# Kernel tuning notes

Measured on AMD Instinct MI355X. Metric: run time of the kernel, lower is better.

The kernel has to match this reference:

```python
import jax, jax.numpy as jnp
import numpy as np

DIM = 1024
HEADS = 16
HEAD_DIM = DIM // HEADS
B, S = 2, 2048


def setup_inputs() -> dict:
    key = jax.random.key(0)
    ks = jax.random.split(key, 12)
    scale = 1.0 / np.sqrt(DIM)
    inp = {
        "Q_in": jax.random.normal(ks[0], (B, S, DIM), jnp.float32),
        "K_in": jax.random.normal(ks[1], (B, S, DIM), jnp.float32),
        "V_in": jax.random.normal(ks[2], (B, S, DIM), jnp.float32),
        "Wq": jax.random.normal(ks[3], (DIM, DIM), jnp.float32) * scale,
        "bq": jnp.zeros((DIM,), jnp.float32),
        "Wk": jax.random.normal(ks[4], (DIM, DIM), jnp.float32) * scale,
        "bk": jnp.zeros((DIM,), jnp.float32),
        "Wv": jax.random.normal(ks[5], (DIM, DIM), jnp.float32) * scale,
        "bv": jnp.zeros((DIM,), jnp.float32),
        "Wo": jax.random.normal(ks[6], (DIM, DIM), jnp.float32) * scale,
        "bo": jnp.zeros((DIM,), jnp.float32),
        "is_causal": 1,
    }
    return inp


def reference(Q_in, K_in, V_in, Wq, bq, Wk, bk, Wv, bv, Wo, bo, is_causal):
    b, s, d = Q_in.shape
    hd = d // HEADS
    # linear projections (torch nn.Linear: x @ W.T + b), split heads -> [b,h,s,hd]
    Q = (Q_in @ Wq.T + bq).reshape(b, s, HEADS, hd).transpose(0, 2, 1, 3)
    K = (K_in @ Wk.T + bk).reshape(b, s, HEADS, hd).transpose(0, 2, 1, 3)
    V = (V_in @ Wv.T + bv).reshape(b, s, HEADS, hd).transpose(0, 2, 1, 3)
    # full [b,h,s,s] score matrix, as in the original (no fused SDPA)
    scores = jnp.einsum("bhqd,bhkd->bhqk", Q, K) / jnp.sqrt(jnp.float32(hd))
    if is_causal:
        causal = jnp.tril(jnp.ones((s, s), dtype=bool))  # [s,s]
        scores = jnp.where(causal, scores, jnp.float32(-jnp.inf))
    attn = jax.nn.softmax(scores, axis=-1)
    # dropout is identity (eval mode) for a deterministic reference
    out = jnp.einsum("bhqk,bhkd->bhqd", attn, V)
    out = out.transpose(0, 2, 1, 3).reshape(b, s, d)
    return out @ Wo.T + bo
```

## Files before the change

kernel.cpp:

```cpp
#include <hip/hip_runtime.h>
#include <hip/hip_bf16.h>
#include <stdint.h>

#define HEADS 16
#define HD 64
#define BATCH 2
#define SEQ 2048
#define NDIM 1024
#define MROWS (BATCH * SEQ)

typedef __attribute__((ext_vector_type(8))) __bf16 bf16x8;
typedef __attribute__((ext_vector_type(4))) __bf16 bf16x4;
typedef __attribute__((ext_vector_type(4))) float f32x4;

#define LOG2E 1.4426950408889634f
#define SOFTMAX_C 16.0f

#if __has_builtin(__builtin_amdgcn_exp2f)
#define EXP2(x) __builtin_amdgcn_exp2f(x)
#else
#define EXP2(x) exp2f(x)
#endif

#define GLDS16(g, l)                                                          \
  __builtin_amdgcn_global_load_lds(                                           \
      (const __attribute__((address_space(1))) unsigned int*)(g),             \
      (__attribute__((address_space(3))) unsigned int*)(l), 16, 0, 0)

__global__ void cvt_all_kernel(const float* __restrict__ xq, const float* __restrict__ xk,
                               const float* __restrict__ xv, const float* __restrict__ wq,
                               const float* __restrict__ wk, const float* __restrict__ wv,
                               const float* __restrict__ wo,
                               __bf16* __restrict__ oxq, __bf16* __restrict__ oxk,
                               __bf16* __restrict__ oxv, __bf16* __restrict__ owq,
                               __bf16* __restrict__ owk, __bf16* __restrict__ owv,
                               __bf16* __restrict__ owo) {
  const int id = blockIdx.x;
  const float* in;
  __bf16* out;
  int blk;
  if (id < 12288) {
    const int m = id >> 12;
    blk = id & 4095;
    in = (m == 0) ? xq : (m == 1) ? xk : xv;
    out = (m == 0) ? oxq : (m == 1) ? oxk : oxv;
  } else {
    const int m = (id - 12288) >> 10;
    blk = (id - 12288) & 1023;
    in = (m == 0) ? wq : (m == 1) ? wk : (m == 2) ? wv : wo;
    out = (m == 0) ? owq : (m == 1) ? owk : (m == 2) ? owv : owo;
  }
  const size_t i = ((size_t)blk * 256 + threadIdx.x) * 4;
  const float4 v = *(const float4*)(in + i);
  bf16x4 o = {(__bf16)v.x, (__bf16)v.y, (__bf16)v.z, (__bf16)v.w};
  *(bf16x4*)(out + i) = o;
}

template <int BNF, bool TRC>
__device__ __forceinline__ void gemm_core(const __bf16* __restrict__ A,
                                          const __bf16* __restrict__ B,
                                          int m0, int n0,
                                          char* lA, char* lB,
                                          f32x4 acc[4][BNF]) {
  constexpr int BBUF = BNF * 2048;
  constexpr int NLD = (BNF == 4) ? 4 : 3;
  const int t = threadIdx.x;
  const int lane = t & 63;
  const int llo = lane & 15, lhi = lane >> 4;
  const int wid = t >> 6;
  const int wrow = (wid >> 1) * 64;
  const int wcol = (wid & 1) * (BNF * 16);

  const int sl = (t & 7) ^ ((t >> 3) & 7);
  const int srg = 2 * (t >> 3) + (sl >> 2);
  const int cg = (sl & 3) * 8;

  const __bf16* pA0 = A + (size_t)(m0 + srg) * 1024 + cg;
  const __bf16* pA1 = A + (size_t)(m0 + 64 + srg) * 1024 + cg;
  const __bf16* pB0 = B + (size_t)(n0 + srg) * 1024 + cg;
  const __bf16* pB1 = B + (size_t)(n0 + (BNF == 4 ? 64 : 0) + srg) * 1024 + cg;

#pragma unroll
  for (int mf = 0; mf < 4; ++mf)
#pragma unroll
    for (int nf = 0; nf < BNF; ++nf)
      acc[mf][nf] = (f32x4){0.f, 0.f, 0.f, 0.f};

#define STAGE_G(buf, k0)                                                      \
  do {                                                                        \
    GLDS16(pA0 + (k0), lA + (buf) * 8192 + t * 16);                           \
    GLDS16(pA1 + (k0), lA + (buf) * 8192 + 4096 + t * 16);                    \
    GLDS16(pB0 + (k0), lB + (buf) * BBUF + t * 16);                           \
    if (BNF == 4) GLDS16(pB1 + (k0), lB + (buf) * BBUF + 4096 + t * 16);      \
  } while (0)

  STAGE_G(0, 0);
  STAGE_G(1, 32);

  const int fcol = ((((llo & 1) << 2) | lhi) ^ (llo >> 1)) << 4;

  int cb = 0;
  for (int k0 = 0; k0 < 1024; k0 += 32) {
    const int step = k0 >> 5;
    if (step + 2 < 32) {
      const int sb = (cb >= 1) ? (cb - 1) : (cb + 2);
      STAGE_G(sb, k0 + 64);
      asm volatile("s_waitcnt vmcnt(%0)" :: "i"(2 * NLD) : "memory");
    } else if (step + 1 < 32) {
      asm volatile("s_waitcnt vmcnt(%0)" :: "i"(NLD) : "memory");
    } else {
      asm volatile("s_waitcnt vmcnt(0)" ::: "memory");
    }
    __builtin_amdgcn_s_barrier();
    __builtin_amdgcn_sched_barrier(0);

    bf16x8 af[4], bfr[BNF];
#pragma unroll
    for (int mf = 0; mf < 4; ++mf) {
      const int R = wrow + mf * 16 + llo;
      af[mf] = *(const bf16x8*)(lA + cb * 8192 + (R >> 1) * 128 + fcol);
    }
#pragma unroll
    for (int nf = 0; nf < BNF; ++nf) {
      const int R = wcol + nf * 16 + llo;
      bfr[nf] = *(const bf16x8*)(lB + cb * BBUF + (R >> 1) * 128 + fcol);
    }
    __builtin_amdgcn_s_setprio(1);
#pragma unroll
    for (int mf = 0; mf < 4; ++mf)
#pragma unroll
      for (int nf = 0; nf < BNF; ++nf)
        acc[mf][nf] = TRC
            ? __builtin_amdgcn_mfma_f32_16x16x32_bf16(bfr[nf], af[mf],
                                                      acc[mf][nf], 0, 0, 0)
            : __builtin_amdgcn_mfma_f32_16x16x32_bf16(af[mf], bfr[nf],
                                                      acc[mf][nf], 0, 0, 0);
    __builtin_amdgcn_s_setprio(0);
    __builtin_amdgcn_s_barrier();
    cb = (cb == 2) ? 0 : (cb + 1);
  }
#undef STAGE_G
}

__global__ __launch_bounds__(256, 3)
void qkv_gemm_kernel(const __bf16* __restrict__ Xq, const __bf16* __restrict__ Xk,
                     const __bf16* __restrict__ Xv, const __bf16* __restrict__ Wq,
                     const __bf16* __restrict__ Wk, const __bf16* __restrict__ Wv,
                     const float* __restrict__ bq, const float* __restrict__ bk,
                     const float* __restrict__ bv, __bf16* __restrict__ Qh,
                     __bf16* __restrict__ Kh, __bf16* __restrict__ Vt) {
  __shared__ __align__(16) char ldsA[3 * 8192];
  __shared__ __align__(16) char ldsB[3 * 8192];

  const int lid = blockIdx.x;
  const int xcd = lid & 7, slot = lid >> 3;
  const int y = slot >> 2;
  const int m0 = (xcd * 4 + (slot & 3)) * 128;
  const int mat = y >> 3;
  const int n0 = (y & 7) * 128;

  const __bf16* A = (mat == 0) ? Xq : (mat == 1) ? Xk : Xv;
  const __bf16* B = (mat == 0) ? Wq : (mat == 1) ? Wk : Wv;
  const float* bias = (mat == 0) ? bq : (mat == 1) ? bk : bv;

  const int t = threadIdx.x;
  const int lane = t & 63;
  const int llo = lane & 15, lhi = lane >> 4;
  const int wid = t >> 6;
  const int wrow = (wid >> 1) * 64;
  const int wcol = (wid & 1) * 64;

  f32x4 acc[4][4];
  if (mat < 2) {
    gemm_core<4, true>(A, B, m0, n0, ldsA, ldsB, acc);
    __bf16* dst = (mat == 0) ? Qh : Kh;
    const float qs = (mat == 0) ? (0.125f * LOG2E) : 1.0f;
#pragma unroll
    for (int nf = 0; nf < 4; ++nf) {
      const int cbase = n0 + wcol + nf * 16 + lhi * 4;
      const float4 b4 = *(const float4*)(bias + cbase);
      const int h = cbase >> 6, d0 = cbase & 63;
#pragma unroll
      for (int mf = 0; mf < 4; ++mf) {
        const int sg = m0 + wrow + mf * 16 + llo;
        const int b = sg >> 11, s0 = sg & 2047;
        bf16x4 pk;
        pk[0] = (__bf16)((acc[mf][nf][0] + b4.x) * qs);
        pk[1] = (__bf16)((acc[mf][nf][1] + b4.y) * qs);
        pk[2] = (__bf16)((acc[mf][nf][2] + b4.z) * qs);
        pk[3] = (__bf16)((acc[mf][nf][3] + b4.w) * qs);
        *(bf16x4*)(dst + ((size_t)(b * HEADS + h) * SEQ + s0) * HD + d0) = pk;
      }
    }
  } else {
    gemm_core<4, false>(A, B, m0, n0, ldsA, ldsB, acc);
#pragma unroll
    for (int nf = 0; nf < 4; ++nf) {
      const int cfull = n0 + wcol + nf * 16 + llo;
      const int h = cfull >> 6, d = cfull & 63;
      const float bb = bias[cfull];
#pragma unroll
      for (int mf = 0; mf < 4; ++mf) {
        const int row0 = m0 + wrow + mf * 16 + lhi * 4;
        const int b = row0 >> 11;
        const int s0 = row0 & 2047;
        bf16x4 pk;
#pragma unroll
        for (int j = 0; j < 4; ++j) pk[j] = (__bf16)(acc[mf][nf][j] + bb);
        *(bf16x4*)(Vt + ((size_t)(b * HEADS + h) * HD + d) * SEQ + s0) = pk;
      }
    }
  }
}

__global__ __launch_bounds__(256, 4)
void attn_kernel(const __bf16* __restrict__ Qh, const __bf16* __restrict__ Kh,
                 const __bf16* __restrict__ Vt, __bf16* __restrict__ O,
                 const int* __restrict__ causal_flag) {
  __shared__ __align__(16) __bf16 kbuf[2][64 * 64];
  __shared__ __align__(16) __bf16 vbuf[2][64 * 64];
  __shared__ __align__(16) __bf16 pbuf[4][16 * 64];

  const int t = threadIdx.x;
  const int lane = t & 63;
  const int llo = lane & 15, lhi = lane >> 4;
  const int w = t >> 6;
  const int causal = causal_flag[0];

  const int lid = blockIdx.x;
  const int xcd = lid & 7, slot = lid >> 3;
  const int group = slot >> 5, r = slot & 31;
  const int bh = xcd + 8 * group;
  const int b = bh >> 4, h = bh & 15;
  const int rr = (group >= 2) ? ((r + 8) & 31) : r;
  const int qt = (group & 1) ? (31 - rr) : rr;

  const __bf16* Qb = Qh + (size_t)bh * SEQ * HD;
  const __bf16* Kb = Kh + (size_t)bh * SEQ * HD;
  const __bf16* Vb = Vt + (size_t)bh * HD * SEQ;

  const int sr = t >> 3;
  const int sce = (((t & 7) * 16) ^ ((sr & 7) << 4)) >> 1;
  const int swz = (llo & 7) << 4;

  char* const pw = (char*)&pbuf[w][0];

  const int qw = qt * 64 + w * 16;
  const int nt = causal ? (qt + 1) : (SEQ / 64);

  bf16x8 bQ[2];
#pragma unroll
  for (int ks = 0; ks < 2; ++ks)
    bQ[ks] = *(const bf16x8*)(Qb + (size_t)(qw + llo) * HD + ks * 32 + lhi * 8);

  float lrun = 0.f;
  f32x4 accO[4];
#pragma unroll
  for (int nf = 0; nf < 4; ++nf) accO[nf] = (f32x4){0.f, 0.f, 0.f, 0.f};

  GLDS16(Kb + (size_t)sr * HD + sce,        (char*)&kbuf[0][0] + t * 16);
  GLDS16(Kb + (size_t)(32 + sr) * HD + sce, (char*)&kbuf[0][0] + 4096 + t * 16);
  GLDS16(Vb + (size_t)sr * SEQ + sce,       (char*)&vbuf[0][0] + t * 16);
  GLDS16(Vb + (size_t)(32 + sr) * SEQ + sce,(char*)&vbuf[0][0] + 4096 + t * 16);
  __syncthreads();
  int cur = 0;

  for (int tkv = 0; tkv < nt; ++tkv) {
    if (tkv + 1 < nt) {
      const int k0s = (tkv + 1) * 64;
      char* kd = (char*)&kbuf[cur ^ 1][0];
      char* vd = (char*)&vbuf[cur ^ 1][0];
      GLDS16(Kb + (size_t)(k0s + sr) * HD + sce,        kd + t * 16);
      GLDS16(Kb + (size_t)(k0s + 32 + sr) * HD + sce,   kd + 4096 + t * 16);
      GLDS16(Vb + (size_t)sr * SEQ + k0s + sce,         vd + t * 16);
      GLDS16(Vb + (size_t)(32 + sr) * SEQ + k0s + sce,  vd + 4096 + t * 16);
    }
    const int k0 = tkv * 64;
    const char* kb = (const char*)&kbuf[cur][0];
    const char* vb = (const char*)&vbuf[cur][0];

    f32x4 s[4];
#pragma unroll
    for (int nf = 0; nf < 4; ++nf) s[nf] = (f32x4){0.f, 0.f, 0.f, 0.f};
    __builtin_amdgcn_s_setprio(1);
#pragma unroll
    for (int ks = 0; ks < 2; ++ks)
#pragma unroll
      for (int nf = 0; nf < 4; ++nf) {
        bf16x8 aK = *(const bf16x8*)(kb + (nf * 16 + llo) * 128 +
                                     ((ks * 64 + lhi * 16) ^ swz));
        s[nf] = __builtin_amdgcn_mfma_f32_16x16x32_bf16(aK, bQ[ks], s[nf], 0, 0, 0);
      }
    __builtin_amdgcn_s_setprio(0);

    if (causal && tkv == qt) {
      const int qrow = qw + llo;
#pragma unroll
      for (int nf = 0; nf < 4; ++nf)
#pragma unroll
        for (int j = 0; j < 4; ++j)
          if (k0 + nf * 16 + lhi * 4 + j > qrow) s[nf][j] = -1e30f;
    }

#pragma unroll
    for (int nf = 0; nf < 4; ++nf)
#pragma unroll
      for (int j = 0; j < 4; ++j) {
        const float pv = EXP2(s[nf][j] - SOFTMAX_C);
        s[nf][j] = pv;
        lrun += pv;
      }

#pragma unroll
    for (int nf = 0; nf < 4; ++nf) {
      bf16x4 pk = {(__bf16)s[nf][0], (__bf16)s[nf][1], (__bf16)s[nf][2],
                   (__bf16)s[nf][3]};
      *(bf16x4*)(pw + llo * 128 + ((32 * nf + 8 * lhi) ^ swz)) = pk;
    }
    __builtin_amdgcn_s_setprio(1);
#pragma unroll
    for (int ks2 = 0; ks2 < 2; ++ks2) {
      bf16x8 bP = *(const bf16x8*)(pw + llo * 128 + ((64 * ks2 + 16 * lhi) ^ swz));
#pragma unroll
      for (int nf = 0; nf < 4; ++nf) {
        bf16x8 aV = *(const bf16x8*)(vb + (nf * 16 + llo) * 128 +
                                     ((64 * ks2 + 16 * lhi) ^ swz));
        accO[nf] = __builtin_amdgcn_mfma_f32_16x16x32_bf16(aV, bP, accO[nf], 0, 0, 0);
      }
    }
    __builtin_amdgcn_s_setprio(0);
    __syncthreads();
    cur ^= 1;
  }

  lrun += __shfl_xor(lrun, 16, 64);
  lrun += __shfl_xor(lrun, 32, 64);
  const float linv = 1.f / lrun;
  const int srow = qw + llo;
#pragma unroll
  for (int nf = 0; nf < 4; ++nf) {
    bf16x4 pk;
#pragma unroll
    for (int j = 0; j < 4; ++j) pk[j] = (__bf16)(accO[nf][j] * linv);
    *(bf16x4*)(O + ((size_t)(b * SEQ + srow) * HEADS + h) * HD + nf * 16 +
               lhi * 4) = pk;
  }
}

__global__ __launch_bounds__(256, 4)
void out_gemm_kernel(const __bf16* __restrict__ Oin, const __bf16* __restrict__ Wo,
                     const float* __restrict__ bo, float* __restrict__ out) {
  __shared__ __align__(16) char ldsA[3 * 8192];
  __shared__ __align__(16) char ldsB[3 * 4096];

  const int lid = blockIdx.x;
  const int xcd = lid & 7, slot = lid >> 3;
  const int n0 = (slot >> 2) * 64;
  const int m0 = (xcd * 4 + (slot & 3)) * 128;

  f32x4 acc[4][2];
  gemm_core<2, false>(Oin, Wo, m0, n0, ldsA, ldsB, acc);

  const int t = threadIdx.x;
  const int lane = t & 63;
  const int llo = lane & 15, lhi = lane >> 4;
  const int wid = t >> 6;
  const int wrow = (wid >> 1) * 64;
  const int wcol = (wid & 1) * 32;

#pragma unroll
  for (int nf = 0; nf < 2; ++nf) {
    const int col = n0 + wcol + nf * 16 + llo;
    const float bb = bo[col];
#pragma unroll
    for (int mf = 0; mf < 4; ++mf)
#pragma unroll
      for (int j = 0; j < 4; ++j) {
        const int row = m0 + wrow + mf * 16 + lhi * 4 + j;
        out[(size_t)row * NDIM + col] = acc[mf][nf][j] + bb;
      }
  }
}

extern "C" void kernel_launch(void* const* d_in, const int* in_sizes, int n_in,
                              void* d_out, int out_size, void* d_ws, size_t ws_size,
                              hipStream_t stream) {
  const float* Q_in = (const float*)d_in[0];
  const float* K_in = (const float*)d_in[1];
  const float* V_in = (const float*)d_in[2];
  const float* Wq = (const float*)d_in[3];
  const float* bq = (const float*)d_in[4];
  const float* Wk = (const float*)d_in[5];
  const float* bk = (const float*)d_in[6];
  const float* Wv = (const float*)d_in[7];
  const float* bv = (const float*)d_in[8];
  const float* Wo = (const float*)d_in[9];
  const float* bo = (const float*)d_in[10];
  const int* causal = (const int*)d_in[11];
  float* out = (float*)d_out;

  char* p = (char*)d_ws;
  const size_t SZ_X = (size_t)MROWS * NDIM * 2;
  const size_t SZ_W = (size_t)NDIM * NDIM * 2;
  __bf16* bXq = (__bf16*)p; p += SZ_X;
  __bf16* bXk = (__bf16*)p; p += SZ_X;
  __bf16* bXv = (__bf16*)p; p += SZ_X;
  __bf16* bWq = (__bf16*)p; p += SZ_W;
  __bf16* bWk = (__bf16*)p; p += SZ_W;
  __bf16* bWv = (__bf16*)p; p += SZ_W;
  __bf16* bWo = (__bf16*)p; p += SZ_W;
  __bf16* Qh  = (__bf16*)p; p += SZ_X;
  __bf16* Kh  = (__bf16*)p; p += SZ_X;
  __bf16* Vt  = (__bf16*)p; p += SZ_X;
  __bf16* Obf = (__bf16*)p; p += SZ_X;

  cvt_all_kernel<<<16384, 256, 0, stream>>>(Q_in, K_in, V_in, Wq, Wk, Wv, Wo,
                                            bXq, bXk, bXv, bWq, bWk, bWv, bWo);

  qkv_gemm_kernel<<<768, 256, 0, stream>>>(bXq, bXk, bXv, bWq, bWk, bWv,
                                           bq, bk, bv, Qh, Kh, Vt);
  attn_kernel<<<1024, 256, 0, stream>>>(Qh, Kh, Vt, Obf, causal);
  out_gemm_kernel<<<512, 256, 0, stream>>>(Obf, bWo, bo, out);
}
```

Before: 112.4 us.

## Fuse fp32-to-bf16 activation conversion into QKV GEMM A-tile loading

Removes the standalone conversion of the three fp32 activation tensors. The QKV GEMM now reads fp32 A tiles straight into registers, converts them to bf16 and writes them to LDS, with the register loads software-pipelined one step ahead. Only the weights still go through a separate conversion kernel. This drops a full write and re-read of the bf16 activation copies, but the GEMM now loads twice the A bytes and gives up async global-to-LDS loads for A, which costs registers and adds LDS store work and waits inside the main loop.

```diff
diff --git a/kernel.cpp b/kernel.cpp
--- a/kernel.cpp
+++ b/kernel.cpp
@@ -27,43 +27,28 @@
       (const __attribute__((address_space(1))) unsigned int*)(g),             \
       (__attribute__((address_space(3))) unsigned int*)(l), 16, 0, 0)
 
-__global__ void cvt_all_kernel(const float* __restrict__ xq, const float* __restrict__ xk,
-                               const float* __restrict__ xv, const float* __restrict__ wq,
-                               const float* __restrict__ wk, const float* __restrict__ wv,
-                               const float* __restrict__ wo,
-                               __bf16* __restrict__ oxq, __bf16* __restrict__ oxk,
-                               __bf16* __restrict__ oxv, __bf16* __restrict__ owq,
-                               __bf16* __restrict__ owk, __bf16* __restrict__ owv,
-                               __bf16* __restrict__ owo) {
+__global__ void cvt_w_kernel(const float* __restrict__ wq, const float* __restrict__ wk,
+                             const float* __restrict__ wv, const float* __restrict__ wo,
+                             __bf16* __restrict__ owq, __bf16* __restrict__ owk,
+                             __bf16* __restrict__ owv, __bf16* __restrict__ owo) {
   const int id = blockIdx.x;
-  const float* in;
-  __bf16* out;
-  int blk;
-  if (id < 12288) {
-    const int m = id >> 12;
-    blk = id & 4095;
-    in = (m == 0) ? xq : (m == 1) ? xk : xv;
-    out = (m == 0) ? oxq : (m == 1) ? oxk : oxv;
-  } else {
-    const int m = (id - 12288) >> 10;
-    blk = (id - 12288) & 1023;
-    in = (m == 0) ? wq : (m == 1) ? wk : (m == 2) ? wv : wo;
-    out = (m == 0) ? owq : (m == 1) ? owk : (m == 2) ? owv : owo;
-  }
+  const int m = id >> 10;
+  const int blk = id & 1023;
+  const float* in = (m == 0) ? wq : (m == 1) ? wk : (m == 2) ? wv : wo;
+  __bf16* out = (m == 0) ? owq : (m == 1) ? owk : (m == 2) ? owv : owo;
   const size_t i = ((size_t)blk * 256 + threadIdx.x) * 4;
   const float4 v = *(const float4*)(in + i);
   bf16x4 o = {(__bf16)v.x, (__bf16)v.y, (__bf16)v.z, (__bf16)v.w};
   *(bf16x4*)(out + i) = o;
 }
 
-template <int BNF, bool TRC>
-__device__ __forceinline__ void gemm_core(const __bf16* __restrict__ A,
+template <int BNF, bool TRC, bool AF32>
+__device__ __forceinline__ void gemm_core(const void* __restrict__ Araw,
                                           const __bf16* __restrict__ B,
                                           int m0, int n0,
                                           char* lA, char* lB,
                                           f32x4 acc[4][BNF]) {
   constexpr int BBUF = BNF * 2048;
-  constexpr int NLD = (BNF == 4) ? 4 : 3;
   const int t = threadIdx.x;
   const int lane = t & 63;
   const int llo = lane & 15, lhi = lane >> 4;
@@ -75,8 +60,6 @@
   const int srg = 2 * (t >> 3) + (sl >> 2);
   const int cg = (sl & 3) * 8;
 
-  const __bf16* pA0 = A + (size_t)(m0 + srg) * 1024 + cg;
-  const __bf16* pA1 = A + (size_t)(m0 + 64 + srg) * 1024 + cg;
   const __bf16* pB0 = B + (size_t)(n0 + srg) * 1024 + cg;
   const __bf16* pB1 = B + (size_t)(n0 + (BNF == 4 ? 64 : 0) + srg) * 1024 + cg;
 
@@ -85,6 +68,40 @@
 #pragma unroll
     for (int nf = 0; nf < BNF; ++nf)
       acc[mf][nf] = (f32x4){0.f, 0.f, 0.f, 0.f};
+
+  const int fcol = ((((llo & 1) << 2) | lhi) ^ (llo >> 1)) << 4;
+
+#define DSREAD_MFMA                                                           \
+  do {                                                                        \
+    bf16x8 af[4], bfr[BNF];                                                   \
+    _Pragma("unroll")                                                         \
+    for (int mf = 0; mf < 4; ++mf) {                                          \
+      const int R = wrow + mf * 16 + llo;                                     \
+      af[mf] = *(const bf16x8*)(lA + cb * 8192 + (R >> 1) * 128 + fcol);      \
+    }                                                                         \
+    _Pragma("unroll")                                                         \
+    for (int nf = 0; nf < BNF; ++nf) {                                        \
+      const int R = wcol + nf * 16 + llo;                                     \
+      bfr[nf] = *(const bf16x8*)(lB + cb * BBUF + (R >> 1) * 128 + fcol);     \
+    }                                                                         \
+    __builtin_amdgcn_s_setprio(1);                                            \
+    _Pragma("unroll")                                                         \
+    for (int mf = 0; mf < 4; ++mf)                                            \
+      _Pragma("unroll")                                                       \
+      for (int nf = 0; nf < BNF; ++nf)                                        \
+        acc[mf][nf] = TRC                                                     \
+            ? __builtin_amdgcn_mfma_f32_16x16x32_bf16(bfr[nf], af[mf],        \
+                                                      acc[mf][nf], 0, 0, 0)   \
+            : __builtin_amdgcn_mfma_f32_16x16x32_bf16(af[mf], bfr[nf],        \
+                                                      acc[mf][nf], 0, 0, 0);  \
+    __builtin_amdgcn_s_setprio(0);                                            \
+  } while (0)
+
+  if constexpr (!AF32) {
+    const __bf16* A = (const __bf16*)Araw;
+    constexpr int NLD = (BNF == 4) ? 4 : 3;
+    const __bf16* pA0 = A + (size_t)(m0 + srg) * 1024 + cg;
+    const __bf16* pA1 = A + (size_t)(m0 + 64 + srg) * 1024 + cg;
 
 #define STAGE_G(buf, k0)                                                      \
   do {                                                                        \
@@ -94,57 +111,103 @@
     if (BNF == 4) GLDS16(pB1 + (k0), lB + (buf) * BBUF + 4096 + t * 16);      \
   } while (0)
 
-  STAGE_G(0, 0);
-  STAGE_G(1, 32);
-
-  const int fcol = ((((llo & 1) << 2) | lhi) ^ (llo >> 1)) << 4;
-
-  int cb = 0;
-  for (int k0 = 0; k0 < 1024; k0 += 32) {
-    const int step = k0 >> 5;
-    if (step + 2 < 32) {
-      const int sb = (cb >= 1) ? (cb - 1) : (cb + 2);
-      STAGE_G(sb, k0 + 64);
-      asm volatile("s_waitcnt vmcnt(%0)" :: "i"(2 * NLD) : "memory");
-    } else if (step + 1 < 32) {
-      asm volatile("s_waitcnt vmcnt(%0)" :: "i"(NLD) : "memory");
-    } else {
-      asm volatile("s_waitcnt vmcnt(0)" ::: "memory");
-    }
-    __builtin_amdgcn_s_barrier();
-    __builtin_amdgcn_sched_barrier(0);
-
-    bf16x8 af[4], bfr[BNF];
-#pragma unroll
-    for (int mf = 0; mf < 4; ++mf) {
-      const int R = wrow + mf * 16 + llo;
-      af[mf] = *(const bf16x8*)(lA + cb * 8192 + (R >> 1) * 128 + fcol);
-    }
-#pragma unroll
-    for (int nf = 0; nf < BNF; ++nf) {
-      const int R = wcol + nf * 16 + llo;
-      bfr[nf] = *(const bf16x8*)(lB + cb * BBUF + (R >> 1) * 128 + fcol);
-    }
-    __builtin_amdgcn_s_setprio(1);
-#pragma unroll
-    for (int mf = 0; mf < 4; ++mf)
-#pragma unroll
-      for (int nf = 0; nf < BNF; ++nf)
-        acc[mf][nf] = TRC
-            ? __builtin_amdgcn_mfma_f32_16x16x32_bf16(bfr[nf], af[mf],
-                                                      acc[mf][nf], 0, 0, 0)
-            : __builtin_amdgcn_mfma_f32_16x16x32_bf16(af[mf], bfr[nf],
-                                                      acc[mf][nf], 0, 0, 0);
-    __builtin_amdgcn_s_setprio(0);
-    __builtin_amdgcn_s_barrier();
-    cb = (cb == 2) ? 0 : (cb + 1);
-  }
+    STAGE_G(0, 0);
+    STAGE_G(1, 32);
+
+    int cb = 0;
+    for (int k0 = 0; k0 < 1024; k0 += 32) {
+      const int step = k0 >> 5;
+      if (step + 2 < 32) {
+        const int sb = (cb >= 1) ? (cb - 1) : (cb + 2);
+        STAGE_G(sb, k0 + 64);
+        asm volatile("s_waitcnt vmcnt(%0)" :: "i"(2 * NLD) : "memory");
+      } else if (step + 1 < 32) {
+        asm volatile("s_waitcnt vmcnt(%0)" :: "i"(NLD) : "memory");
+      } else {
+        asm volatile("s_waitcnt vmcnt(0)" ::: "memory");
+      }
+      __builtin_amdgcn_s_barrier();
+      __builtin_amdgcn_sched_barrier(0);
+      DSREAD_MFMA;
+      __builtin_amdgcn_s_barrier();
+      cb = (cb == 2) ? 0 : (cb + 1);
+    }
 #undef STAGE_G
+  } else {
+    const float* fA = (const float*)Araw;
+    const float* fpA0 = fA + (size_t)(m0 + srg) * 1024 + cg;
+    const float* fpA1 = fA + (size_t)(m0 + 64 + srg) * 1024 + cg;
+
+#define STAGEB(buf, k0)                                                       \
+  do {                                                                        \
+    GLDS16(pB0 + (k0), lB + (buf) * BBUF + t * 16);                           \
+    if (BNF == 4) GLDS16(pB1 + (k0), lB + (buf) * BBUF + 4096 + t * 16);      \
+  } while (0)
+
+#define WRITEA(buf, sa, sb_, sc, sd)                                          \
+  do {                                                                        \
+    bf16x8 v0, v1;                                                            \
+    v0[0]=(__bf16)(sa).x; v0[1]=(__bf16)(sa).y; v0[2]=(__bf16)(sa).z; v0[3]=(__bf16)(sa).w; \
+    v0[4]=(__bf16)(sb_).x; v0[5]=(__bf16)(sb_).y; v0[6]=(__bf16)(sb_).z; v0[7]=(__bf16)(sb_).w; \
+    v1[0]=(__bf16)(sc).x; v1[1]=(__bf16)(sc).y; v1[2]=(__bf16)(sc).z; v1[3]=(__bf16)(sc).w; \
+    v1[4]=(__bf16)(sd).x; v1[5]=(__bf16)(sd).y; v1[6]=(__bf16)(sd).z; v1[7]=(__bf16)(sd).w; \
+    *(bf16x8*)(lA + (buf) * 8192 + t * 16) = v0;                              \
+    *(bf16x8*)(lA + (buf) * 8192 + 4096 + t * 16) = v1;                       \
+  } while (0)
+
+    float4 p0a, p0b, p0c, p0d;
+    float4 p1a, p1b, p1c, p1d;
+
+    p0a = *(const float4*)(fpA0 + 0);  p0b = *(const float4*)(fpA0 + 4);
+    p0c = *(const float4*)(fpA1 + 0);  p0d = *(const float4*)(fpA1 + 4);
+    WRITEA(0, p0a, p0b, p0c, p0d);
+    STAGEB(0, 0);
+    STAGEB(1, 32);
+    p1a = *(const float4*)(fpA0 + 32); p1b = *(const float4*)(fpA0 + 36);
+    p1c = *(const float4*)(fpA1 + 32); p1d = *(const float4*)(fpA1 + 36);
+
+    int cb = 0;
+
+#define QSTEP(K0CUR, LA_, LB_, LC_, LD_, WA_, WB_, WC_, WD_)                  \
+  {                                                                           \
+    const int step_ = (K0CUR) >> 5;                                           \
+    const int wb_ = (cb == 2) ? 0 : cb + 1;                                   \
+    const int sb_ = (wb_ == 2) ? 0 : wb_ + 1;                                 \
+    if (step_ + 2 < 32) {                                                     \
+      STAGEB(sb_, (K0CUR) + 64);                                              \
+      LA_ = *(const float4*)(fpA0 + (K0CUR) + 64);                            \
+      LB_ = *(const float4*)(fpA0 + (K0CUR) + 68);                            \
+      LC_ = *(const float4*)(fpA1 + (K0CUR) + 64);                            \
+      LD_ = *(const float4*)(fpA1 + (K0CUR) + 68);                            \
+    }                                                                         \
+    if (step_ + 1 < 32) WRITEA(wb_, WA_, WB_, WC_, WD_);                      \
+    if (step_ + 2 < 32) {                                                     \
+      asm volatile("s_waitcnt vmcnt(6)" ::: "memory");                        \
+    } else {                                                                  \
+      asm volatile("s_waitcnt vmcnt(0)" ::: "memory");                        \
+    }                                                                         \
+    asm volatile("s_waitcnt lgkmcnt(0)" ::: "memory");                        \
+    __builtin_amdgcn_s_barrier();                                             \
+    __builtin_amdgcn_sched_barrier(0);                                        \
+    DSREAD_MFMA;                                                              \
+    __builtin_amdgcn_s_barrier();                                             \
+    cb = (cb == 2) ? 0 : (cb + 1);                                            \
+  }
+
+    for (int k0 = 0; k0 < 1024; k0 += 64) {
+      QSTEP(k0,      p0a, p0b, p0c, p0d,  p1a, p1b, p1c, p1d);
+      QSTEP(k0 + 32, p1a, p1b, p1c, p1d,  p0a, p0b, p0c, p0d);
+    }
+#undef QSTEP
+#undef WRITEA
+#undef STAGEB
+  }
+#undef DSREAD_MFMA
 }
 
 __global__ __launch_bounds__(256, 3)
-void qkv_gemm_kernel(const __bf16* __restrict__ Xq, const __bf16* __restrict__ Xk,
-                     const __bf16* __restrict__ Xv, const __bf16* __restrict__ Wq,
+void qkv_gemm_kernel(const float* __restrict__ Xq, const float* __restrict__ Xk,
+                     const float* __restrict__ Xv, const __bf16* __restrict__ Wq,
                      const __bf16* __restrict__ Wk, const __bf16* __restrict__ Wv,
                      const float* __restrict__ bq, const float* __restrict__ bk,
                      const float* __restrict__ bv, __bf16* __restrict__ Qh,
@@ -159,7 +222,8 @@
   const int mat = y >> 3;
   const int n0 = (y & 7) * 128;
 
-  const __bf16* A = (mat == 0) ? Xq : (mat == 1) ? Xk : Xv;
+  const void* A = (mat == 0) ? (const void*)Xq
+                 : (mat == 1) ? (const void*)Xk : (const void*)Xv;
   const __bf16* B = (mat == 0) ? Wq : (mat == 1) ? Wk : Wv;
   const float* bias = (mat == 0) ? bq : (mat == 1) ? bk : bv;
 
@@ -172,7 +236,7 @@
 
   f32x4 acc[4][4];
   if (mat < 2) {
-    gemm_core<4, true>(A, B, m0, n0, ldsA, ldsB, acc);
+    gemm_core<4, true, true>(A, B, m0, n0, ldsA, ldsB, acc);
     __bf16* dst = (mat == 0) ? Qh : Kh;
     const float qs = (mat == 0) ? (0.125f * LOG2E) : 1.0f;
 #pragma unroll
@@ -193,7 +257,7 @@
       }
     }
   } else {
-    gemm_core<4, false>(A, B, m0, n0, ldsA, ldsB, acc);
+    gemm_core<4, false, true>(A, B, m0, n0, ldsA, ldsB, acc);
 #pragma unroll
     for (int nf = 0; nf < 4; ++nf) {
       const int cfull = n0 + wcol + nf * 16 + llo;
@@ -359,7 +423,7 @@
   const int m0 = (xcd * 4 + (slot & 3)) * 128;
 
   f32x4 acc[4][2];
-  gemm_core<2, false>(Oin, Wo, m0, n0, ldsA, ldsB, acc);
+  gemm_core<2, false, false>((const void*)Oin, Wo, m0, n0, ldsA, ldsB, acc);
 
   const int t = threadIdx.x;
   const int lane = t & 63;
@@ -402,9 +466,6 @@
   char* p = (char*)d_ws;
   const size_t SZ_X = (size_t)MROWS * NDIM * 2;
   const size_t SZ_W = (size_t)NDIM * NDIM * 2;
-  __bf16* bXq = (__bf16*)p; p += SZ_X;
-  __bf16* bXk = (__bf16*)p; p += SZ_X;
-  __bf16* bXv = (__bf16*)p; p += SZ_X;
   __bf16* bWq = (__bf16*)p; p += SZ_W;
   __bf16* bWk = (__bf16*)p; p += SZ_W;
   __bf16* bWv = (__bf16*)p; p += SZ_W;
@@ -414,10 +475,9 @@
   __bf16* Vt  = (__bf16*)p; p += SZ_X;
   __bf16* Obf = (__bf16*)p; p += SZ_X;
 
-  cvt_all_kernel<<<16384, 256, 0, stream>>>(Q_in, K_in, V_in, Wq, Wk, Wv, Wo,
-                                            bXq, bXk, bXv, bWq, bWk, bWv, bWo);
-
-  qkv_gemm_kernel<<<768, 256, 0, stream>>>(bXq, bXk, bXv, bWq, bWk, bWv,
+  cvt_w_kernel<<<4096, 256, 0, stream>>>(Wq, Wk, Wv, Wo, bWq, bWk, bWv, bWo);
+
+  qkv_gemm_kernel<<<768, 256, 0, stream>>>(Q_in, K_in, V_in, bWq, bWk, bWv,
                                            bq, bk, bv, Qh, Kh, Vt);
   attn_kernel<<<1024, 256, 0, stream>>>(Qh, Kh, Vt, Obf, causal);
   out_gemm_kernel<<<512, 256, 0, stream>>>(Obf, bWo, bo, out);
```

Result: faster. 107.4 us (median of 2 runs) (-4.4%).
